# Kernel tuning notes

Measured on AMD Instinct MI355X. Metric: run time of the kernel, lower is better.

Reference implementation:

```python
import math
import jax, jax.numpy as jnp
from jax import lax
import numpy as np

N_IMG = 2
C = 128
IMG_H, IMG_W = 512, 1024
STRIDES = (4, 8, 16, 32, 64)
SIZES = (32.0, 64.0, 128.0, 256.0, 512.0)
RATIOS = (0.5, 1.0, 2.0)
A = len(RATIOS)
PRE_NMS_TOPK = 2000    # pre_nms_topk[self.training] with training=True
POST_NMS_TOPK = 1000   # post_nms_topk[self.training]
NMS_THRESH = 0.7
BATCH_PER_IMG = 256
POS_FRAC = 0.5
MIN_BOX_SIZE = 0.0
SCALE_CLAMP = math.log(1000.0 / 16.0)
MATCH_LOW, MATCH_HIGH = 0.3, 0.7


def cell_anchors(size):
    rs = jnp.asarray(RATIOS, jnp.float32)
    area = size * size
    w = jnp.sqrt(area / rs)
    h = w * rs
    return jnp.stack([-w / 2, -h / 2, w / 2, h / 2], axis=1)  # [A,4]


def level_anchors(H, W, stride, size):
    ca = cell_anchors(size)
    sx = jnp.arange(W, dtype=jnp.float32) * stride
    sy = jnp.arange(H, dtype=jnp.float32) * stride
    yy, xx = jnp.meshgrid(sy, sx, indexing="ij")
    shifts = jnp.stack([xx, yy, xx, yy], axis=-1).reshape(-1, 4)  # [H*W,4]
    return (shifts[:, None, :] + ca[None, :, :]).reshape(-1, 4)  # [H*W*A,4]


def pairwise_iou(a, b):
    lt = jnp.maximum(a[:, None, :2], b[None, :, :2])
    rb = jnp.minimum(a[:, None, 2:], b[None, :, 2:])
    wh = jnp.clip(rb - lt, 0.0)
    inter = wh[..., 0] * wh[..., 1]
    area_a = (a[:, 2] - a[:, 0]) * (a[:, 3] - a[:, 1])
    area_b = (b[:, 2] - b[:, 0]) * (b[:, 3] - b[:, 1])
    union = area_a[:, None] + area_b[None, :] - inter
    return jnp.where(inter > 0, inter / union, 0.0)


def get_deltas(src, tgt):
    sw = src[..., 2] - src[..., 0]; sh = src[..., 3] - src[..., 1]
    scx = src[..., 0] + 0.5 * sw;   scy = src[..., 1] + 0.5 * sh
    tw = tgt[..., 2] - tgt[..., 0]; th = tgt[..., 3] - tgt[..., 1]
    tcx = tgt[..., 0] + 0.5 * tw;   tcy = tgt[..., 1] + 0.5 * th
    return jnp.stack([(tcx - scx) / sw, (tcy - scy) / sh,
                      jnp.log(tw / sw), jnp.log(th / sh)], axis=-1)


def apply_deltas(deltas, boxes):
    w = boxes[..., 2] - boxes[..., 0]; h = boxes[..., 3] - boxes[..., 1]
    cx = boxes[..., 0] + 0.5 * w;      cy = boxes[..., 1] + 0.5 * h
    dx, dy = deltas[..., 0], deltas[..., 1]
    dw = jnp.minimum(deltas[..., 2], SCALE_CLAMP)
    dh = jnp.minimum(deltas[..., 3], SCALE_CLAMP)
    pcx = dx * w + cx; pcy = dy * h + cy
    pw = jnp.exp(dw) * w; ph = jnp.exp(dh) * h
    return jnp.stack([pcx - 0.5 * pw, pcy - 0.5 * ph,
                      pcx + 0.5 * pw, pcy + 0.5 * ph], axis=-1)


def conv(x, w, b):
    y = lax.conv_general_dilated(x, w, (1, 1), "SAME",
                                 dimension_numbers=("NCHW", "OIHW", "NCHW"))
    return y + b[None, :, None, None]


def rpn_forward_flat(feats, conv_w, conv_b, obj_w, obj_b, delta_w, delta_b):
    anchors, logits, deltas = [], [], []
    for (stride, size), f in zip(zip(STRIDES, SIZES), feats):
        N, _, H, W = f.shape
        h = jax.nn.relu(conv(f, conv_w, conv_b))
        lg = conv(h, obj_w, obj_b)       # [N,A,H,W]
        dl = conv(h, delta_w, delta_b)   # [N,4A,H,W]
        logits.append(lg.transpose(0, 2, 3, 1).reshape(N, -1))                     # [N,HWA]
        deltas.append(dl.reshape(N, A, 4, H, W).transpose(0, 3, 4, 1, 2).reshape(N, -1, 4))
        anchors.append(level_anchors(H, W, stride, size))
    return anchors, logits, deltas


def label_and_sample(gt_b, key, anchors_all):
    iou = pairwise_iou(gt_b, anchors_all)                 # [G,R]
    matched_idxs = jnp.argmax(iou, axis=0)
    matched_vals = jnp.max(iou, axis=0)
    labels = jnp.where(matched_vals >= MATCH_HIGH, 1,
             jnp.where(matched_vals >= MATCH_LOW, -1, 0))
    highest = jnp.max(iou, axis=1)                        # per-gt best IoU
    lq = jnp.any((iou == highest[:, None]) & (highest[:, None] > 0), axis=0)
    labels = jnp.where(lq, 1, labels)                     # allow_low_quality_matches
    R = labels.shape[0]
    kf, kb = jax.random.split(key)
    fg = labels == 1; bg = labels == 0
    num_fg = jnp.minimum(fg.sum(), int(POS_FRAC * BATCH_PER_IMG))
    num_bg = jnp.minimum(bg.sum(), BATCH_PER_IMG - num_fg)
    def pick(mask, k, num):
        pri = jnp.where(mask, jax.random.uniform(k, (R,)), jnp.inf)
        rank = jnp.argsort(jnp.argsort(pri))
        return rank < num
    sel_fg = pick(fg, kf, num_fg)
    sel_bg = pick(bg, kb, num_bg)
    labels = jnp.where(sel_fg, 1, jnp.where(sel_bg, 0, -1))
    return labels, gt_b[matched_idxs]


def losses_fn(anchors_all, logits_cat, deltas_cat, gt_labels, matched_gt):
    fg = (gt_labels == 1).astype(logits_cat.dtype)          # [N,R]
    gt_deltas = get_deltas(anchors_all[None], matched_gt)   # [N,R,4]
    loc = jnp.sum(jnp.abs(deltas_cat - gt_deltas) * fg[..., None])  # smooth_l1, beta=0
    valid = (gt_labels >= 0).astype(logits_cat.dtype)
    x = logits_cat
    bce = jnp.maximum(x, 0.0) - x * fg + jnp.log1p(jnp.exp(-jnp.abs(x)))
    cls = jnp.sum(bce * valid)
    norm = float(BATCH_PER_IMG) * logits_cat.shape[0]
    return jnp.stack([cls / norm, loc / norm])


def nms_keep(boxes, valid):
    # boxes are sorted by descending score; greedy suppression.
    K = boxes.shape[0]
    iou = pairwise_iou(boxes, boxes)
    idx = jnp.arange(K)
    def body(i, keep):
        sup = (iou[i] > NMS_THRESH) & (idx > i) & keep[i]
        return keep & ~sup
    return lax.fori_loop(0, K, body, valid)


def predict_proposals(anchors, logits, deltas):
    lvl_boxes, lvl_scores = [], []
    for anc, lg, dl in zip(anchors, logits, deltas):
        boxes = apply_deltas(dl, anc[None])             # [N,R_l,4]
        k = min(PRE_NMS_TOPK, lg.shape[1])
        ts, ti = lax.top_k(lg, k)                       # [N,k]
        tb = jnp.take_along_axis(boxes, ti[..., None], axis=1)
        tb = jnp.stack([jnp.clip(tb[..., 0], 0.0, IMG_W), jnp.clip(tb[..., 1], 0.0, IMG_H),
                        jnp.clip(tb[..., 2], 0.0, IMG_W), jnp.clip(tb[..., 3], 0.0, IMG_H)], -1)
        valid = ((tb[..., 2] - tb[..., 0]) > MIN_BOX_SIZE) & ((tb[..., 3] - tb[..., 1]) > MIN_BOX_SIZE)
        keep = jax.vmap(nms_keep)(tb, valid)
        lvl_boxes.append(tb)
        lvl_scores.append(jnp.where(keep, ts, -jnp.inf))
    all_b = jnp.concatenate(lvl_boxes, axis=1)
    all_s = jnp.concatenate(lvl_scores, axis=1)
    fs, fi = lax.top_k(all_s, POST_NMS_TOPK)
    fb = jnp.take_along_axis(all_b, fi[..., None], axis=1)
    return fb, fs


def setup_inputs() -> dict:
    key = jax.random.key(0)
    ks = jax.random.split(key, 12)
    out = {}
    for i, s in enumerate(STRIDES):
        out[f"feat_p{i+2}"] = jax.random.normal(ks[i], (N_IMG, C, IMG_H // s, IMG_W // s), jnp.float32)
    G = 32
    wh_scale = jnp.asarray([IMG_W, IMG_H], jnp.float32)
    cxy = jax.random.uniform(ks[5], (N_IMG, G, 2)) * wh_scale
    wh = 32.0 + jax.random.uniform(ks[6], (N_IMG, G, 2)) * 224.0
    x1y1 = jnp.clip(cxy - wh / 2, 0.0)
    x2y2 = jnp.maximum(jnp.minimum(cxy + wh / 2, wh_scale), x1y1 + 1.0)
    out["gt_boxes"] = jnp.concatenate([x1y1, x2y2], axis=-1)
    out["conv_w"] = 0.01 * jax.random.normal(ks[7], (C, C, 3, 3), jnp.float32)
    out["conv_b"] = jnp.zeros((C,), jnp.float32)
    out["obj_w"] = 0.01 * jax.random.normal(ks[8], (A, C, 1, 1), jnp.float32)
    out["obj_b"] = jnp.zeros((A,), jnp.float32)
    out["delta_w"] = 0.01 * jax.random.normal(ks[9], (4 * A, C, 1, 1), jnp.float32)
    out["delta_b"] = jnp.zeros((4 * A,), jnp.float32)
    return out


def reference(feat_p2, feat_p3, feat_p4, feat_p5, feat_p6, gt_boxes,
              conv_w, conv_b, obj_w, obj_b, delta_w, delta_b):
    feats = [feat_p2, feat_p3, feat_p4, feat_p5, feat_p6]
    anchors, logits, deltas = rpn_forward_flat(feats, conv_w, conv_b, obj_w, obj_b, delta_w, delta_b)
    anchors_all = jnp.concatenate(anchors, axis=0)      # [R,4]
    logits_cat = jnp.concatenate(logits, axis=1)        # [N,R]
    deltas_cat = jnp.concatenate(deltas, axis=1)        # [N,R,4]
    keys = jax.random.split(jax.random.key(42), gt_boxes.shape[0])
    gt_labels, matched_gt = jax.vmap(label_and_sample, in_axes=(0, 0, None))(gt_boxes, keys, anchors_all)
    losses = losses_fn(anchors_all, logits_cat, deltas_cat, gt_labels, matched_gt)
    prop_boxes, prop_scores = predict_proposals(
        anchors,
        [lax.stop_gradient(l) for l in logits],
        [lax.stop_gradient(d) for d in deltas])
    return prop_boxes, prop_scores, losses
```

## Files before the change

### kernel.cpp

```cpp
#include <hip/hip_runtime.h>
#include <stdint.h>
#include <math.h>


#define R_TOT   130944
#define HALF_R  65472
#define TOTK    7920
#define SCALE_CLAMP 4.135166556742356

__host__ __device__ inline void threefry(uint32_t k0, uint32_t k1,
                                         uint32_t x0, uint32_t x1,
                                         uint32_t* o0, uint32_t* o1)
{
  uint32_t ks[3]; ks[0]=k0; ks[1]=k1; ks[2]=k0^k1^0x1BD11BDAu;
  x0 += ks[0]; x1 += ks[1];
  const uint32_t rot0[4] = {13u,15u,26u,6u};
  const uint32_t rot1[4] = {17u,29u,16u,24u};
  for (int i = 0; i < 5; i++){
    const uint32_t* rot = (i & 1) ? rot1 : rot0;
    for (int q = 0; q < 4; q++){
      x0 += x1;
      x1 = (x1 << rot[q]) | (x1 >> (32u - rot[q]));
      x1 ^= x0;
    }
    x0 += ks[(i+1)%3];
    x1 += ks[(i+2)%3] + (uint32_t)(i+1);
  }
  *o0 = x0; *o1 = x1;
}

__device__ inline unsigned long long mono64(double v){
  unsigned long long b = (unsigned long long)__double_as_longlong(v);
  return (b & 0x8000000000000000ull) ? ~b : (b | 0x8000000000000000ull);
}

__device__ __forceinline__ double iou_cf(double g0,double g1,double g2,double g3,
                                         double a0,double a1,double a2,double a3){
  #pragma clang fp contract(off)
  double lt0 = fmax(g0,a0), lt1 = fmax(g1,a1);
  double rb0 = fmin(g2,a2), rb1 = fmin(g3,a3);
  double w = rb0-lt0; if (w<0.0) w=0.0;
  double h = rb1-lt1; if (h<0.0) h=0.0;
  double inter = w*h;
  double aa = (g2-g0)*(g3-g1);
  double ab = (a2-a0)*(a3-a1);
  double uni = aa+ab-inter;
  return inter>0.0 ? inter/uni : 0.0;
}

__device__ __forceinline__ void anchor_of(int r, double* o){
  #pragma clang fp contract(off)
  const int    base[5]={0,98304,122880,129024,130560};
  const int    Wl[5]  ={256,128,64,32,16};
  const double strd[5]={4.0,8.0,16.0,32.0,64.0};
  const double size[5]={32.0,64.0,128.0,256.0,512.0};
  const double ratio[3]={0.5,1.0,2.0};
  int l=0; while (l<4 && r>=base[l+1]) l++;
  int rr=r-base[l]; int pix=rr/3; int a=rr-pix*3;
  int x=pix%Wl[l], y=pix/Wl[l];
  double w=sqrt(size[l]*size[l]/ratio[a]);
  double h=w*ratio[a];
  double sx=(double)x*strd[l], sy=(double)y*strd[l];
  o[0]=sx-0.5*w; o[1]=sy-0.5*h; o[2]=sx+0.5*w; o[3]=sy+0.5*h;
}

__device__ __forceinline__ void decode_box(int ridx, const double* __restrict__ d,
                                           double* __restrict__ o){
  double a[4]; anchor_of(ridx,a);
  double w=a[2]-a[0], h=a[3]-a[1];
  double cx=a[0]+0.5*w, cy=a[1]+0.5*h;
  double dw=fmin(d[2],SCALE_CLAMP), dh=fmin(d[3],SCALE_CLAMP);
  double pcx=d[0]*w+cx, pcy=d[1]*h+cy;
  double pw=exp(dw)*w, ph=exp(dh)*h;
  double x1=pcx-0.5*pw, y1=pcy-0.5*ph;
  double x2=pcx+0.5*pw, y2=pcy+0.5*ph;
  o[0]=fmin(fmax(x1,0.0),1024.0); o[1]=fmin(fmax(y1,0.0),512.0);
  o[2]=fmin(fmax(x2,0.0),1024.0); o[3]=fmin(fmax(y2,0.0),512.0);
}

__device__ inline void bitonic_desc(double* sv, int* si, int M, int tid, int nthr){
  for (int k=2;k<=M;k<<=1)
    for (int j=k>>1;j>0;j>>=1){
      __syncthreads();
      for (int i=tid;i<M;i+=nthr){
        int ixj=i^j;
        if (ixj>i){
          double va=sv[i], vb=sv[ixj]; int ia=si[i], ib=si[ixj];
          bool before = (va>vb) || (va==vb && ia<ib);
          bool up = ((i&k)==0);
          if (up ? !before : before){ sv[i]=vb; sv[ixj]=va; si[i]=ib; si[ixj]=ia; }
        }
      }
    }
  __syncthreads();
}

__device__ inline void bitonic_asc_u(uint32_t* sk, int* si, int M, int tid, int nthr){
  for (int k=2;k<=M;k<<=1)
    for (int j=k>>1;j>0;j>>=1){
      __syncthreads();
      for (int i=tid;i<M;i+=nthr){
        int ixj=i^j;
        if (ixj>i){
          uint32_t ka=sk[i], kb=sk[ixj]; int ia=si[i], ib=si[ixj];
          bool before = (ka<kb) || (ka==kb && ia<ib);
          bool up = ((i&k)==0);
          if (up ? !before : before){ sk[i]=kb; sk[ixj]=ka; si[i]=ib; si[ixj]=ia; }
        }
      }
    }
  __syncthreads();
}

__global__ __launch_bounds__(256) void k_pre(const float* __restrict__ cw,
    float* __restrict__ cwTf, const float* __restrict__ gt,
    unsigned long long* __restrict__ highest)
{
  const int bx=blockIdx.x, tid=threadIdx.x;
  if (bx < 768){
    int o = bx*256 + tid;
    if (o >= 147456) return;
    int cc = o / 1152; int rem = o - cc*1152;
    int ci = rem / 9;  int k9 = rem - ci*9;
    cwTf[((size_t)cc*128 + ci)*12 + k9] = cw[o];
  } else {
    __shared__ double gts[128];
    __shared__ unsigned long long lmax[32];
    const int gb=bx-768;
    const int img=gb>>6, b=gb&63;
    if (tid<128) gts[tid]=(double)gt[img*128+tid];
    if (tid<32) lmax[tid]=0ull;
    __syncthreads();
    double gm[32];
    #pragma unroll
    for (int g=0;g<32;g++) gm[g]=0.0;
    for (int r=b*256+tid; r<R_TOT; r+=64*256){
      double a[4]; anchor_of(r,a);
      #pragma unroll
      for (int g=0;g<32;g++){
        double v=iou_cf(gts[g*4],gts[g*4+1],gts[g*4+2],gts[g*4+3],a[0],a[1],a[2],a[3]);
        gm[g]=fmax(gm[g],v);
      }
    }
    #pragma unroll
    for (int g=0;g<32;g++){
      double v=gm[g];
      #pragma unroll
      for (int off=1; off<64; off<<=1) v=fmax(v,__shfl_xor(v,off));
      if ((tid&63)==0) atomicMax(&lmax[g],(unsigned long long)__double_as_longlong(v));
    }
    __syncthreads();
    if (tid<32) atomicMax(&highest[img*32+tid], lmax[tid]);
  }
}

#define CTH 4
#define CTW 8

__global__ __launch_bounds__(256,4) void k_conv_label(
    const float* __restrict__ f2, const float* __restrict__ f3,
    const float* __restrict__ f4, const float* __restrict__ f5,
    const float* __restrict__ f6,
    const float* __restrict__ cwTf, const float* __restrict__ cb,
    const float* __restrict__ ow, const float* __restrict__ ob,
    const float* __restrict__ dwt, const float* __restrict__ dbt,
    double* __restrict__ logits, double* __restrict__ dpred,
    const float* __restrict__ gt, const unsigned long long* __restrict__ highest,
    int* __restrict__ prelab, int* __restrict__ matched,
    int* __restrict__ labels, int* __restrict__ counts,
    uint32_t* __restrict__ ub,
    uint32_t kf00,uint32_t kf01,uint32_t kb00,uint32_t kb01,
    uint32_t kf10,uint32_t kf11,uint32_t kb10,uint32_t kb11)
{
  __shared__ double fshd[4][6][12];
  __shared__ __align__(16) char ush[17408];
  double* hshp = (double*)ush;
  __shared__ float hw[15*128];
  __shared__ float hb[15];

  const int tid=threadIdx.x;

  if (blockIdx.x >= 3752){
    int j = (blockIdx.x-3752)*256 + tid;
    if (j >= 2*R_TOT) return;
    int slot = j / HALF_R; int t = j - slot*HALF_R;
    uint32_t k0,k1;
    if      (slot==0){k0=kf00;k1=kf01;}
    else if (slot==1){k0=kb00;k1=kb01;}
    else if (slot==2){k0=kf10;k1=kf11;}
    else             {k0=kb10;k1=kb11;}
    uint32_t o0,o1;
    threefry(k0,k1,(uint32_t)t,(uint32_t)(t+HALF_R),&o0,&o1);
    ub[(size_t)slot*R_TOT+t]=o0;
    ub[(size_t)slot*R_TOT+t+HALF_R]=o1;
    return;
  }

  if (blockIdx.x >= 2728){
    double* gts=(double*)ush;
    double* hg =(double*)(ush+1024);
    int* wfg=(int*)(ush+1280); int* wbg=(int*)(ush+1296);
    const int lb=blockIdx.x-2728;
    const int img=lb>>9, blk=lb&511;
    if (tid<128) gts[tid]=(double)gt[img*128+tid];
    if (tid<32)  hg[tid]=__longlong_as_double((long long)highest[img*32+tid]);
    __syncthreads();
    int r=blk*256+tid;
    const bool ok=(r<R_TOT);
    int lab=-1, bi=0;
    if (ok){
      double a[4]; anchor_of(r,a);
      double best=-1.0; bool lq=false;
      #pragma unroll
      for (int g=0;g<32;g++){
        double v=iou_cf(gts[g*4],gts[g*4+1],gts[g*4+2],gts[g*4+3],a[0],a[1],a[2],a[3]);
        if (v>best){ best=v; bi=g; }
        if (hg[g]>0.0 && v==hg[g]) lq=true;
      }
      lab = lq ? 1 : (best>=0.7 ? 1 : (best>=0.3 ? -1 : 0));
      prelab [(size_t)img*R_TOT+r]=lab;
      matched[(size_t)img*R_TOT+r]=bi;
      labels [(size_t)img*R_TOT+r]=-1;
    }
    unsigned long long bf=__ballot(ok && lab==1);
    unsigned long long bb=__ballot(ok && lab==0);
    const int wid=tid>>6, lane=tid&63;
    if (lane==0){ wfg[wid]=__popcll(bf); wbg[wid]=__popcll(bb); }
    __syncthreads();
    if (tid==0){
      int fcnt=wfg[0]+wfg[1]+wfg[2]+wfg[3];
      int bcnt=wbg[0]+wbg[1]+wbg[2]+wbg[3];
      if (fcnt) atomicAdd(&counts[img*2+0],fcnt);
      if (bcnt) atomicAdd(&counts[img*2+1],bcnt);
    }
    return;
  }

  const int cumt[6]={0,2048,2560,2688,2720,2728};
  const int Hs[5]={128,64,32,16,8}, Wl[5]={256,128,64,32,16};
  const int rbs[5]={0,98304,122880,129024,130560};
  const int lgx[5]={5,4,3,2,1};

  int bid=blockIdx.x;
  int lvl=0;
  while (lvl<4 && bid>=cumt[lvl+1]) lvl++;
  int t=bid-cumt[lvl];
  const int img=t&1; const int tt=t>>1;
  const int H=Hs[lvl], W=Wl[lvl], rbase=rbs[lvl];
  const int tx=tt&((1<<lgx[lvl])-1), ty=tt>>lgx[lvl];
  const int x0=tx*CTW, y0=ty*CTH;
  const float* f = lvl==0?f2: lvl==1?f3: lvl==2?f4: lvl==3?f5: f6;

  for (int i=tid;i<15*128;i+=256){
    int o=i>>7, c=i&127;
    hw[i]=(o<3)?ow[o*128+c]:dwt[(o-3)*128+c];
  }
  if (tid<15) hb[tid]=(tid<3)?ob[tid]:dbt[tid-3];

  const int c=tid&127, half=tid>>7;
  double acc[16];
  #pragma unroll
  for (int i=0;i<16;i++) acc[i]=0.0;

  const float* fimg = f + (size_t)img*128*H*W;
  const float* wbase = cwTf + (size_t)c*1536;

  const bool fin_act = (tid < 240);
  int ci_f=0,dy_f=0,dx_f=0; bool fin_valid=false;
  const float* fptr=fimg;
  if (fin_act){
    ci_f=tid/60; int rem=tid-ci_f*60; dy_f=rem/10; dx_f=rem-dy_f*10;
    int y=y0-1+dy_f, x=x0-1+dx_f;
    fin_valid = (y>=0&&y<H&&x>=0&&x<W);
    fptr = fimg + (size_t)ci_f*H*W + (fin_valid ? ((size_t)y*W+x) : 0);
  }
  const size_t fstep=(size_t)4*H*W;

  float fin_pf=0.f;
  if (fin_act){ fin_pf = fin_valid ? *fptr : 0.f; fptr += fstep; }

  for (int ci0=0; ci0<128; ci0+=4){
    __syncthreads();
    if (fin_act) fshd[ci_f][dy_f][dx_f]=(double)fin_pf;
    if (ci0+4<128){
      if (fin_act){ fin_pf = fin_valid ? *fptr : 0.f; fptr += fstep; }
    }
    __syncthreads();
    #pragma unroll
    for (int ci=0;ci<4;ci++){
      const float4* wp=(const float4*)(wbase + (size_t)(ci0+ci)*12);
      float4 wA=wp[0], wB=wp[1], wC=wp[2];
      double w9d[9];
      w9d[0]=(double)wA.x; w9d[1]=(double)wA.y; w9d[2]=(double)wA.z; w9d[3]=(double)wA.w;
      w9d[4]=(double)wB.x; w9d[5]=(double)wB.y; w9d[6]=(double)wB.z; w9d[7]=(double)wB.w;
      w9d[8]=(double)wC.x;
      #pragma unroll
      for (int irl=0;irl<4;irl++){
        int ir=half*2+irl;
        double rowb[10];
        #pragma unroll
        for (int q=0;q<10;q++) rowb[q]=fshd[ci][ir][q];
        #pragma unroll
        for (int orl=0;orl<2;orl++){
          int ky=irl-orl;
          if (ky<0||ky>2) continue;
          #pragma unroll
          for (int px=0;px<8;px++){
            double s=acc[orl*8+px];
            #pragma unroll
            for (int kx=0;kx<3;kx++) s += w9d[ky*3+kx]*rowb[px+kx];
            acc[orl*8+px]=s;
          }
        }
      }
    }
  }
  double bc=(double)cb[c];
  __syncthreads();
  if (half==0){
    #pragma unroll
    for (int pp=0;pp<16;pp++){
      double hv=acc[pp]+bc; if (hv<0.0) hv=0.0;
      hshp[c*17+pp]=hv;
    }
  }
  __syncthreads();
  for (int hp=0;hp<2;hp++){
    if (tid<240){
      int o=tid>>4, p=tid&15;
      double s=(double)hb[o];
      for (int c2=0;c2<128;c2++) s += (double)hw[o*128+c2]*hshp[c2*17+p];
      int pg=hp*16+p;
      int py=pg>>3, px=pg&7;
      int gy=y0+py, gx=x0+px;
      long long pix=(long long)gy*W+gx;
      size_t rb=(size_t)rbase+(size_t)pix*3;
      if (o<3) logits[(size_t)img*R_TOT+rb+o]=s;
      else { int a=(o-3)>>2, jj=(o-3)&3; dpred[((size_t)img*R_TOT+rb+a)*4+jj]=s; }
    }
    if (hp==0){
      __syncthreads();
      if (half==1){
        #pragma unroll
        for (int pp=0;pp<16;pp++){
          double hv=acc[pp]+bc; if (hv<0.0) hv=0.0;
          hshp[c*17+pp]=hv;
        }
      }
      __syncthreads();
    }
  }
}

__global__ __launch_bounds__(1024) void k_mid2(const uint32_t* __restrict__ ub,
    const int* __restrict__ prelab, const int* __restrict__ counts,
    int* __restrict__ labels,
    const double* __restrict__ logits, const double* __restrict__ dpred,
    double* __restrict__ allS, double* __restrict__ allB)
{
  __shared__ __align__(16) char buf[49152];
  __shared__ int hist[256];
  __shared__ int sI0, sI1; __shared__ unsigned long long sT;
  __shared__ int cnt;
  const int tid=threadIdx.x;

  if (blockIdx.x < 4){
    uint32_t* skey=(uint32_t*)buf; int* sidx=(int*)(buf+16384);
    const int img=blockIdx.x>>1, cls=blockIdx.x&1;
    const int cfg=counts[img*2+0], cbg=counts[img*2+1];
    const int num_fg=cfg<128?cfg:128;
    const int cap_bg=256-num_fg;
    const int num=cls?(cbg<cap_bg?cbg:cap_bg):num_fg;
    if (num<=0) return;
    const int want=cls?0:1;
    const int sel=want;
    const uint32_t* u=ub+(size_t)(img*2+cls)*R_TOT;
    const int* pl=prelab+(size_t)img*R_TOT;
    int* lab=labels+(size_t)img*R_TOT;

    for (int b=tid;b<256;b+=1024) hist[b]=0;
    if (tid==0) cnt=0;
    __syncthreads();
    for (int r=tid;r<R_TOT;r+=1024){
      int plr = pl[r];
      uint32_t key = u[r]>>9;
      if (plr==want) atomicAdd(&hist[key>>15],1);
    }
    __syncthreads();
    if (tid==0){
      int cum=0,b=0;
      for (;b<255;b++){ int hh=hist[b]; if (cum+hh>=num) break; cum+=hh; }
      sI0=b; sI1=num-cum;
    }
    __syncthreads();
    const uint32_t bsel=(uint32_t)sI0; const int kneed=sI1;
    for (int r=tid;r<R_TOT;r+=1024){
      int plr = pl[r];
      uint32_t key = u[r]>>9;
      if (plr==want){
        uint32_t t8=key>>15;
        if (t8<bsel) lab[r]=sel;
        else if (t8==bsel){ int p=atomicAdd(&cnt,1); if (p<4096){ skey[p]=key; sidx[p]=r; } }
      }
    }
    __syncthreads();
    int n=cnt<4096?cnt:4096;
    for (int i=tid;i<4096;i+=1024) if (i>=n){ skey[i]=0xFFFFFFFFu; sidx[i]=0x7FFFFFFF; }
    bitonic_asc_u(skey,sidx,4096,tid,1024);
    int take = kneed<n?kneed:n;
    for (int i=tid;i<take;i+=1024) lab[sidx[i]]=sel;
  } else {
    double* sv=(double*)buf; int* si=(int*)(buf+32768);
    const int Rl[5]   ={98304,24576,6144,1536,384};
    const int kl[5]   ={2000,2000,2000,1536,384};
    const int lbase[5]={0,98304,122880,129024,130560};
    const int loff[5] ={0,2000,4000,6000,7536};
    const int bb=blockIdx.x-4;
    const int lvl=bb%5, img=bb/5;
    const int Rn=Rl[lvl], K=kl[lvl];
    const double* lg=logits+(size_t)img*R_TOT+lbase[lvl];

    unsigned long long chosen=0; int kneed=K;
    for (int ps=7; ps>=6; --ps){
      int shift=ps*8;
      for (int b=tid;b<256;b+=1024) hist[b]=0;
      __syncthreads();
      for (int r=tid;r<Rn;r+=1024){
        unsigned long long ik=~mono64(lg[r]);
        bool okp=(ps==7)||((ik>>(shift+8))==(chosen>>(shift+8)));
        if (okp) atomicAdd(&hist[(int)((ik>>shift)&255)],1);
      }
      __syncthreads();
      if (tid==0){
        int cum=0,b=0;
        for (;b<255;b++){ int hh=hist[b]; if (cum+hh>=kneed) break; cum+=hh; }
        sT=chosen|((unsigned long long)b<<shift); sI1=kneed-cum;
      }
      __syncthreads();
      chosen=sT; kneed=sI1;
      __syncthreads();
    }
    const unsigned long long lim = chosen | 0xFFFFFFFFFFFFull;
    if (tid==0) cnt=0;
    __syncthreads();
    for (int r=tid;r<Rn;r+=1024){
      unsigned long long ik=~mono64(lg[r]);
      if (ik<=lim){ int p=atomicAdd(&cnt,1); if (p<4096){ sv[p]=lg[r]; si[p]=r; } }
    }
    __syncthreads();
    int n=cnt<4096?cnt:4096;
    for (int i=tid;i<4096;i+=1024) if (i>=n){ sv[i]=-HUGE_VAL; si[i]=0x7FFFFFFF; }
    bitonic_desc(sv,si,4096,tid,1024);
    for (int j=tid;j<K;j+=1024){
      double v=sv[j]; int r=si[j];
      size_t slot=(size_t)img*TOTK+loff[lvl]+j;
      allS[slot]=v;
      int ridx=lbase[lvl]+r;
      double bx[4];
      decode_box(ridx, dpred+((size_t)img*R_TOT+ridx)*4, bx);
      allB[slot*4+0]=bx[0]; allB[slot*4+1]=bx[1]; allB[slot*4+2]=bx[2]; allB[slot*4+3]=bx[3];
    }
  }
}

__global__ __launch_bounds__(256) void k_mid3(const double* __restrict__ allB,
    unsigned long long* __restrict__ msk,
    const double* __restrict__ logits, const double* __restrict__ dpred,
    const float* __restrict__ gt, const int* __restrict__ labels,
    const int* __restrict__ matched, double* __restrict__ part)
{
  const int bx=blockIdx.x, tid=threadIdx.x;
  if (bx < 1980){
    __shared__ double Bsh[8000];
    const int kl[5]  ={2000,2000,2000,1536,384};
    const int loff[5]={0,2000,4000,6000,7536};
    const int rbc[6] ={0,250,500,750,942,990};
    const int img = bx/990; int t = bx - img*990;
    int lvl=0; while (lvl<4 && t>=rbc[lvl+1]) lvl++;
    const int i0=(t-rbc[lvl])*8;
    const int K=kl[lvl]; const int nw=(K+63)>>6;
    const double* B=allB+(size_t)(img*TOTK+loff[lvl])*4;
    for (int q=tid;q<K*4;q+=256) Bsh[q]=B[q];
    __syncthreads();
    const int wv=tid>>6, lane=tid&63;
    for (int rr=0;rr<8;rr++){
      int i=i0+rr;
      if (i>=K) break;
      const double bi0=Bsh[i*4],bi1=Bsh[i*4+1],bi2=Bsh[i*4+2],bi3=Bsh[i*4+3];
      const double areai=(bi2-bi0)*(bi3-bi1);
      for (int w=wv;w<nw;w+=4){
        int j=w*64+lane;
        bool pred=false;
        if (j<K && j>i){
          double a0=Bsh[j*4],a1=Bsh[j*4+1],a2=Bsh[j*4+2],a3=Bsh[j*4+3];
          double lt0=fmax(bi0,a0), lt1=fmax(bi1,a1);
          double rb0=fmin(bi2,a2), rb1=fmin(bi3,a3);
          double ww=rb0-lt0; if (ww<0.0) ww=0.0;
          double hh=rb1-lt1; if (hh<0.0) hh=0.0;
          double inter=ww*hh;
          double uni=areai+(a2-a0)*(a3-a1)-inter;
          double iou=inter>0.0?inter/uni:0.0;
          pred = iou>0.7;
        }
        unsigned long long m=__ballot(pred);
        if (lane==0) msk[((size_t)img*TOTK+loff[lvl]+i)*32+w]=m;
      }
    }
  } else {
    const int bid2=bx-1980;
    double cls=0.0, loc=0.0;
    for (int idx=bid2*256+tid; idx<2*R_TOT; idx+=256*256){
      int l=labels[idx];
      if (l<0) continue;
      double x=logits[idx];
      double fgv=(l==1)?1.0:0.0;
      cls += fmax(x,0.0)-x*fgv+log1p(exp(-fabs(x)));
      if (l==1){
        int img=idx/R_TOT, r=idx-img*R_TOT;
        double a[4]; anchor_of(r,a);
        int m=matched[idx];
        const float* g=gt+img*128+m*4;
        double sw=a[2]-a[0], sh=a[3]-a[1];
        double scx=a[0]+0.5*sw, scy=a[1]+0.5*sh;
        double tw=(double)g[2]-(double)g[0], th=(double)g[3]-(double)g[1];
        double tcx=(double)g[0]+0.5*tw, tcy=(double)g[1]+0.5*th;
        double d0=(tcx-scx)/sw, d1=(tcy-scy)/sh;
        double d2=log(tw/sw), d3=log(th/sh);
        const double* dp=dpred+(size_t)idx*4;
        loc += fabs(dp[0]-d0)+fabs(dp[1]-d1)+fabs(dp[2]-d2)+fabs(dp[3]-d3);
      }
    }
    __shared__ double sc[256], sl[256];
    sc[tid]=cls; sl[tid]=loc; __syncthreads();
    for (int s=128;s>0;s>>=1){
      if (tid<s){ sc[tid]+=sc[tid+s]; sl[tid]+=sl[tid+s]; }
      __syncthreads();
    }
    if (tid==0){ part[bid2*2]=sc[0]; part[bid2*2+1]=sl[0]; }
  }
}

#define NMS_LD(BUF, BASE) do{ \
  _Pragma("unroll") \
  for (int j_=0;j_<16;j_++){ int i_=(BASE)+j_; \
    BUF[j_] = (lane<nw && i_<K) ? M[(size_t)i_*32+lane] : 0ull; } \
}while(0)
#define NMS_PR(BUF, BASE) do{ \
  _Pragma("unroll") \
  for (int j_=0;j_<16;j_++){ int i_=(BASE)+j_; \
    if (i_<K){ unsigned long long kw_=__shfl(keep,(i_>>6)); \
      if ((kw_>>(i_&63))&1ull) keep &= ~BUF[j_]; } } \
}while(0)

__global__ void k_nmsscan(const double* __restrict__ allB, double* __restrict__ allS,
    const unsigned long long* __restrict__ msk){
  const int kl[5]  ={2000,2000,2000,1536,384};
  const int loff[5]={0,2000,4000,6000,7536};
  const int lvl=blockIdx.x, img=blockIdx.y;
  const int K=kl[lvl], off=loff[lvl], nw=(K+63)>>6;
  const int lane=threadIdx.x;
  const double* B=allB+(size_t)(img*TOTK+off)*4;
  const unsigned long long* M=msk+((size_t)img*TOTK+off)*32;
  unsigned long long keep=0ull;
  if (lane<nw){
    for (int b=0;b<64;b++){
      int j=lane*64+b;
      if (j<K){
        double x1=B[(size_t)j*4],y1=B[(size_t)j*4+1],x2=B[(size_t)j*4+2],y2=B[(size_t)j*4+3];
        if ((x2-x1)>0.0 && (y2-y1)>0.0) keep|=(1ull<<b);
      }
    }
  }
  unsigned long long Abuf[16], Bbuf[16];
  NMS_LD(Abuf, 0);
  for (int base=0; base<K; base+=32){
    NMS_LD(Bbuf, base+16);
    NMS_PR(Abuf, base);
    NMS_LD(Abuf, base+32);
    NMS_PR(Bbuf, base+16);
  }
  if (lane<nw){
    for (int b=0;b<64;b++){
      int j=lane*64+b;
      if (j<K && !((keep>>b)&1ull))
        allS[(size_t)img*TOTK+off+j]=-HUGE_VAL;
    }
  }
}

__global__ __launch_bounds__(1024) void k_final(const double* __restrict__ allS,
    const double* __restrict__ allB, const double* __restrict__ part,
    float* __restrict__ out){
  const int tid=threadIdx.x;
  if (blockIdx.x==2){
    __shared__ double sc[256], sl[256];
    if (tid<256){ sc[tid]=part[tid*2]; sl[tid]=part[tid*2+1]; }
    __syncthreads();
    for (int s=128;s>0;s>>=1){
      if (tid<s){ sc[tid]+=sc[tid+s]; sl[tid]+=sl[tid+s]; }
      __syncthreads();
    }
    if (tid==0){ out[10000]=(float)(sc[0]/512.0); out[10001]=(float)(sl[0]/512.0); }
    return;
  }
  const int img=blockIdx.x;
  const double* sarr=allS+(size_t)img*TOTK;
  __shared__ int hist[256];
  __shared__ unsigned long long sT; __shared__ int sK;
  __shared__ double sv[4096]; __shared__ int si[4096]; __shared__ int cnt;

  unsigned long long chosen=0; int kneed=1000;
  for (int ps=7; ps>=0; --ps){
    int shift=ps*8;
    for (int b=tid;b<256;b+=1024) hist[b]=0;
    __syncthreads();
    for (int r=tid;r<TOTK;r+=1024){
      unsigned long long ik=~mono64(sarr[r]);
      bool okp=(ps==7)||((ik>>(shift+8))==(chosen>>(shift+8)));
      if (okp) atomicAdd(&hist[(int)((ik>>shift)&255)],1);
    }
    __syncthreads();
    if (tid==0){
      int cum=0,b=0;
      for (;b<255;b++){ int hh=hist[b]; if (cum+hh>=kneed) break; cum+=hh; }
      sT=chosen|((unsigned long long)b<<shift); sK=kneed-cum;
    }
    __syncthreads();
    chosen=sT; kneed=sK;
    __syncthreads();
  }
  if (tid==0) cnt=0;
  __syncthreads();
  for (int r=tid;r<TOTK;r+=1024){
    unsigned long long ik=~mono64(sarr[r]);
    if (ik<=chosen){ int p=atomicAdd(&cnt,1); if (p<4096){ sv[p]=sarr[r]; si[p]=r; } }
  }
  __syncthreads();
  int n=cnt<4096?cnt:4096;
  for (int i=tid;i<4096;i+=1024) if (i>=n){ sv[i]=-HUGE_VAL; si[i]=0x7FFFFFFF; }
  bitonic_desc(sv,si,4096,tid,1024);
  for (int j=tid;j<1000;j+=1024){
    out[8000+img*1000+j]=(float)sv[j];
    int idx=si[j];
    const double* b=allB+((size_t)img*TOTK+idx)*4;
    float* ob=out+((size_t)img*1000+j)*4;
    ob[0]=(float)b[0]; ob[1]=(float)b[1]; ob[2]=(float)b[2]; ob[3]=(float)b[3];
  }
}

extern "C" void kernel_launch(void* const* d_in, const int* in_sizes, int n_in,
                              void* d_out, int out_size, void* d_ws, size_t ws_size,
                              hipStream_t stream)
{
  (void)in_sizes; (void)n_in; (void)out_size;
  const float* feats[5];
  for (int i=0;i<5;i++) feats[i]=(const float*)d_in[i];
  const float* gt =(const float*)d_in[5];
  const float* cw =(const float*)d_in[6];
  const float* cb =(const float*)d_in[7];
  const float* ow =(const float*)d_in[8];
  const float* ob =(const float*)d_in[9];
  const float* dwt=(const float*)d_in[10];
  const float* dbt=(const float*)d_in[11];
  float* out=(float*)d_out;

  char* p=(char*)d_ws;
  auto carve=[&](size_t nbytes)->char*{ char* q=p; p += (nbytes+255)&~(size_t)255; return q; };
  double* logits =(double*)carve(2ull*R_TOT*8);
  double* dpred  =(double*)carve(2ull*R_TOT*4*8);
  float* cwTf    =(float*)carve(128ull*128*12*4);
  uint32_t* ub   =(uint32_t*)carve(4ull*R_TOT*4);
  int* prelab    =(int*)carve(2ull*R_TOT*4);
  int* matched   =(int*)carve(2ull*R_TOT*4);
  int* labels    =(int*)carve(2ull*R_TOT*4);
  unsigned long long* highest=(unsigned long long*)carve(2*32*8);
  int* counts    =(int*)carve(256);
  double* allS   =(double*)carve(2ull*TOTK*8);
  double* allB   =(double*)carve(2ull*TOTK*4*8);
  unsigned long long* msk=(unsigned long long*)carve(2ull*TOTK*32*8);
  double* part   =(double*)carve(256*2*8);
  if ((size_t)(p-(char*)d_ws) > ws_size) return;

  hipMemsetAsync(highest, 0, 768, stream);

  uint32_t a0,b0,a1,b1;
  threefry(0u,42u,0u,2u,&a0,&b0);
  threefry(0u,42u,1u,3u,&a1,&b1);
  uint32_t kf00,kf01,kb00,kb01,kf10,kf11,kb10,kb11;
  { uint32_t c0,d0,c1,d1;
    threefry(a0,a1,0u,2u,&c0,&d0); threefry(a0,a1,1u,3u,&c1,&d1);
    kf00=c0; kf01=c1; kb00=d0; kb01=d1;
    threefry(b0,b1,0u,2u,&c0,&d0); threefry(b0,b1,1u,3u,&c1,&d1);
    kf10=c0; kf11=c1; kb10=d0; kb11=d1; }

  k_pre<<<896, 256, 0, stream>>>(cw, cwTf, gt, highest);
  k_conv_label<<<4775, 256, 0, stream>>>(feats[0],feats[1],feats[2],feats[3],feats[4],
      cwTf,cb,ow,ob,dwt,dbt, logits, dpred,
      gt, highest, prelab, matched, labels, counts,
      ub, kf00,kf01,kb00,kb01,kf10,kf11,kb10,kb11);
  k_mid2<<<14, 1024, 0, stream>>>(ub, prelab, counts, labels, logits, dpred, allS, allB);
  k_mid3<<<2236, 256, 0, stream>>>(allB, msk, logits, dpred, gt, labels, matched, part);
  k_nmsscan<<<dim3(5,2), 64, 0, stream>>>(allB, allS, msk);
  k_final<<<3, 1024, 0, stream>>>(allS, allB, part, out);
}
```

Measured before the change: 1.467 ms.

## Stage conv weights in shared memory, parallelize histogram selection, shorten final radix select

The 3x3 conv weights are re-laid out as [ci][k][cout] and each 4-channel chunk is staged cooperatively into shared memory with register prefetch, replacing per-thread strided global loads. The shared buffer grows and the occupancy hint rises from 4 to 5 blocks per SM. The serial single-thread histogram scan in the top-k selection becomes a parallel prefix sum. The final top-1000 radix select now stops after two byte passes and keeps everything under a coarse threshold, relying on the bitonic sort buffer to absorb the extra candidates. If more than 4096 candidates pass, the truncation could change results.

```diff
diff --git a/kernel.cpp b/kernel.cpp
--- a/kernel.cpp
+++ b/kernel.cpp
@@ -112,21 +112,38 @@
   __syncthreads();
 }
 
+__device__ inline void hist_select(int* hist, int kneed, int tid,
+                                   int* shb, int* shk){
+  for (int off=1; off<256; off<<=1){
+    int v=0;
+    if (tid<256 && tid>=off) v=hist[tid-off];
+    __syncthreads();
+    if (tid<256) hist[tid]+=v;
+    __syncthreads();
+  }
+  if (tid<256){
+    int prev = tid ? hist[tid-1] : 0;
+    if (prev < kneed && kneed <= hist[tid]){ *shb=tid; *shk=kneed-prev; }
+    if (tid==255 && kneed > hist[255]){ *shb=255; *shk=kneed-hist[254]; }
+  }
+  __syncthreads();
+}
+
 __global__ __launch_bounds__(256) void k_pre(const float* __restrict__ cw,
     float* __restrict__ cwTf, const float* __restrict__ gt,
     unsigned long long* __restrict__ highest)
 {
   const int bx=blockIdx.x, tid=threadIdx.x;
-  if (bx < 768){
+  if (bx < 576){
     int o = bx*256 + tid;
     if (o >= 147456) return;
-    int cc = o / 1152; int rem = o - cc*1152;
-    int ci = rem / 9;  int k9 = rem - ci*9;
-    cwTf[((size_t)cc*128 + ci)*12 + k9] = cw[o];
+    int cc = o & 127; int t = o >> 7;
+    int k9 = t % 9;  int ci = t / 9;
+    cwTf[(size_t)(ci*9+k9)*128 + cc] = cw[(size_t)cc*1152 + ci*9 + k9];
   } else {
     __shared__ double gts[128];
     __shared__ unsigned long long lmax[32];
-    const int gb=bx-768;
+    const int gb=bx-576;
     const int img=gb>>6, b=gb&63;
     if (tid<128) gts[tid]=(double)gt[img*128+tid];
     if (tid<32) lmax[tid]=0ull;
@@ -157,7 +174,7 @@
 #define CTH 4
 #define CTW 8
 
-__global__ __launch_bounds__(256,4) void k_conv_label(
+__global__ __launch_bounds__(256,5) void k_conv_label(
     const float* __restrict__ f2, const float* __restrict__ f3,
     const float* __restrict__ f4, const float* __restrict__ f5,
     const float* __restrict__ f6,
@@ -173,7 +190,8 @@
     uint32_t kf10,uint32_t kf11,uint32_t kb10,uint32_t kb11)
 {
   __shared__ double fshd[4][6][12];
-  __shared__ __align__(16) char ush[17408];
+  __shared__ __align__(16) char ush[18432];
+  float*  wshF = (float*)ush;
   double* hshp = (double*)ush;
   __shared__ float hw[15*128];
   __shared__ float hb[15];
@@ -263,7 +281,6 @@
   for (int i=0;i<16;i++) acc[i]=0.0;
 
   const float* fimg = f + (size_t)img*128*H*W;
-  const float* wbase = cwTf + (size_t)c*1536;
 
   const bool fin_act = (tid < 240);
   int ci_f=0,dy_f=0,dx_f=0; bool fin_valid=false;
@@ -275,25 +292,31 @@
     fptr = fimg + (size_t)ci_f*H*W + (fin_valid ? ((size_t)y*W+x) : 0);
   }
   const size_t fstep=(size_t)4*H*W;
-
-  float fin_pf=0.f;
+  const float2* wsrc=(const float2*)cwTf;
+
+  float fin_pf=0.f; float2 wpf[9];
   if (fin_act){ fin_pf = fin_valid ? *fptr : 0.f; fptr += fstep; }
+  #pragma unroll
+  for (int j2=0;j2<9;j2++) wpf[j2]=wsrc[tid+j2*256];
 
   for (int ci0=0; ci0<128; ci0+=4){
     __syncthreads();
     if (fin_act) fshd[ci_f][dy_f][dx_f]=(double)fin_pf;
+    { float2* wdst=(float2*)wshF;
+      #pragma unroll
+      for (int j2=0;j2<9;j2++) wdst[tid+j2*256]=wpf[j2]; }
     if (ci0+4<128){
       if (fin_act){ fin_pf = fin_valid ? *fptr : 0.f; fptr += fstep; }
+      const float2* wn = wsrc + (size_t)(ci0+4)*576;
+      #pragma unroll
+      for (int j2=0;j2<9;j2++) wpf[j2]=wn[tid+j2*256];
     }
     __syncthreads();
     #pragma unroll
     for (int ci=0;ci<4;ci++){
-      const float4* wp=(const float4*)(wbase + (size_t)(ci0+ci)*12);
-      float4 wA=wp[0], wB=wp[1], wC=wp[2];
       double w9d[9];
-      w9d[0]=(double)wA.x; w9d[1]=(double)wA.y; w9d[2]=(double)wA.z; w9d[3]=(double)wA.w;
-      w9d[4]=(double)wB.x; w9d[5]=(double)wB.y; w9d[6]=(double)wB.z; w9d[7]=(double)wB.w;
-      w9d[8]=(double)wC.x;
+      #pragma unroll
+      for (int k=0;k<9;k++) w9d[k]=(double)wshF[(ci*9+k)*128 + c];
       #pragma unroll
       for (int irl=0;irl<4;irl++){
         int ir=half*2+irl;
@@ -360,7 +383,7 @@
 {
   __shared__ __align__(16) char buf[49152];
   __shared__ int hist[256];
-  __shared__ int sI0, sI1; __shared__ unsigned long long sT;
+  __shared__ int sI0, sI1;
   __shared__ int cnt;
   const int tid=threadIdx.x;
 
@@ -387,12 +410,7 @@
       if (plr==want) atomicAdd(&hist[key>>15],1);
     }
     __syncthreads();
-    if (tid==0){
-      int cum=0,b=0;
-      for (;b<255;b++){ int hh=hist[b]; if (cum+hh>=num) break; cum+=hh; }
-      sI0=b; sI1=num-cum;
-    }
-    __syncthreads();
+    hist_select(hist, num, tid, &sI0, &sI1);
     const uint32_t bsel=(uint32_t)sI0; const int kneed=sI1;
     for (int r=tid;r<R_TOT;r+=1024){
       int plr = pl[r];
@@ -431,13 +449,9 @@
         if (okp) atomicAdd(&hist[(int)((ik>>shift)&255)],1);
       }
       __syncthreads();
-      if (tid==0){
-        int cum=0,b=0;
-        for (;b<255;b++){ int hh=hist[b]; if (cum+hh>=kneed) break; cum+=hh; }
-        sT=chosen|((unsigned long long)b<<shift); sI1=kneed-cum;
-      }
-      __syncthreads();
-      chosen=sT; kneed=sI1;
+      hist_select(hist, kneed, tid, &sI0, &sI1);
+      chosen = chosen | ((unsigned long long)sI0<<shift);
+      kneed  = sI1;
       __syncthreads();
     }
     const unsigned long long lim = chosen | 0xFFFFFFFFFFFFull;
@@ -606,11 +620,11 @@
   const int img=blockIdx.x;
   const double* sarr=allS+(size_t)img*TOTK;
   __shared__ int hist[256];
-  __shared__ unsigned long long sT; __shared__ int sK;
+  __shared__ int sI0, sI1;
   __shared__ double sv[4096]; __shared__ int si[4096]; __shared__ int cnt;
 
   unsigned long long chosen=0; int kneed=1000;
-  for (int ps=7; ps>=0; --ps){
+  for (int ps=7; ps>=6; --ps){
     int shift=ps*8;
     for (int b=tid;b<256;b+=1024) hist[b]=0;
     __syncthreads();
@@ -620,20 +634,17 @@
       if (okp) atomicAdd(&hist[(int)((ik>>shift)&255)],1);
     }
     __syncthreads();
-    if (tid==0){
-      int cum=0,b=0;
-      for (;b<255;b++){ int hh=hist[b]; if (cum+hh>=kneed) break; cum+=hh; }
-      sT=chosen|((unsigned long long)b<<shift); sK=kneed-cum;
-    }
-    __syncthreads();
-    chosen=sT; kneed=sK;
-    __syncthreads();
-  }
+    hist_select(hist, kneed, tid, &sI0, &sI1);
+    chosen = chosen | ((unsigned long long)sI0<<shift);
+    kneed  = sI1;
+    __syncthreads();
+  }
+  const unsigned long long lim = chosen | 0xFFFFFFFFFFFFull;
   if (tid==0) cnt=0;
   __syncthreads();
   for (int r=tid;r<TOTK;r+=1024){
     unsigned long long ik=~mono64(sarr[r]);
-    if (ik<=chosen){ int p=atomicAdd(&cnt,1); if (p<4096){ sv[p]=sarr[r]; si[p]=r; } }
+    if (ik<=lim){ int p=atomicAdd(&cnt,1); if (p<4096){ sv[p]=sarr[r]; si[p]=r; } }
   }
   __syncthreads();
   int n=cnt<4096?cnt:4096;
@@ -668,7 +679,7 @@
   auto carve=[&](size_t nbytes)->char*{ char* q=p; p += (nbytes+255)&~(size_t)255; return q; };
   double* logits =(double*)carve(2ull*R_TOT*8);
   double* dpred  =(double*)carve(2ull*R_TOT*4*8);
-  float* cwTf    =(float*)carve(128ull*128*12*4);
+  float* cwTf    =(float*)carve(147456ull*4);
   uint32_t* ub   =(uint32_t*)carve(4ull*R_TOT*4);
   int* prelab    =(int*)carve(2ull*R_TOT*4);
   int* matched   =(int*)carve(2ull*R_TOT*4);
@@ -693,7 +704,7 @@
     threefry(b0,b1,0u,2u,&c0,&d0); threefry(b0,b1,1u,3u,&c1,&d1);
     kf10=c0; kf11=c1; kb10=d0; kb11=d1; }
 
-  k_pre<<<896, 256, 0, stream>>>(cw, cwTf, gt, highest);
+  k_pre<<<704, 256, 0, stream>>>(cw, cwTf, gt, highest);
   k_conv_label<<<4775, 256, 0, stream>>>(feats[0],feats[1],feats[2],feats[3],feats[4],
       cwTf,cb,ow,ob,dwt,dbt, logits, dpred,
       gt, highest, prelab, matched, labels, counts,
```

Result: faster. 1.354 ms (-7.7%).
